# Kernel tuning notes

Hardware: AMD Instinct MI355X
Metric: run time of the kernel (lower is better)

Reference implementation:

```python
import jax, jax.numpy as jnp
import numpy as np
from jax import lax

B, T_CAP, V, WD, H, L, IC = 256, 51, 10000, 512, 512, 2, 2048


def setup_inputs() -> dict:
    key = jax.random.key(0)
    ks = jax.random.split(key, 16)
    u01 = lambda k, s: jax.random.uniform(k, s, jnp.float32, -0.1, 0.1)
    sc = 1.0 / np.sqrt(H)
    uh = lambda k, s: jax.random.uniform(k, s, jnp.float32, -sc, sc)
    image_code = jax.random.normal(ks[0], (B, IC), jnp.float32)
    captions = jax.random.randint(ks[1], (B, T_CAP), 0, V)
    cap_lens = jax.random.randint(ks[2], (B,), 2, T_CAP + 1)
    cap_lens = cap_lens.at[0].set(T_CAP)  # guarantees max len == T_CAP (static scan length)
    return {
        "image_code": image_code,
        "captions": captions,
        "cap_lens": cap_lens,
        "embed_w": u01(ks[3], (V, WD)),
        "init_w": uh(ks[4], (L * H, IC)),
        "init_b": uh(ks[5], (L * H,)),
        "w_ih0": uh(ks[6], (3 * H, WD + IC)),
        "w_hh0": uh(ks[7], (3 * H, H)),
        "b_ih0": uh(ks[8], (3 * H,)),
        "b_hh0": uh(ks[9], (3 * H,)),
        "w_ih1": uh(ks[10], (3 * H, H)),
        "w_hh1": uh(ks[11], (3 * H, H)),
        "b_ih1": uh(ks[12], (3 * H,)),
        "b_hh1": uh(ks[13], (3 * H,)),
        "fc_w": u01(ks[14], (V, H)),
        "fc_b": jnp.zeros((V,), jnp.float32),
    }


def _gru_cell(x, h, w_ih, w_hh, b_ih, b_hh):
    # torch nn.GRU cell: gates ordered (r, z, n)
    gi = x @ w_ih.T + b_ih
    gh = h @ w_hh.T + b_hh
    i_r, i_z, i_n = jnp.split(gi, 3, axis=-1)
    h_r, h_z, h_n = jnp.split(gh, 3, axis=-1)
    r = jax.nn.sigmoid(i_r + h_r)
    z = jax.nn.sigmoid(i_z + h_z)
    n = jnp.tanh(i_n + r * h_n)
    return (1.0 - z) * n + z * h


def reference(image_code, captions, cap_lens, embed_w, init_w, init_b,
              w_ih0, w_hh0, b_ih0, b_hh0, w_ih1, w_hh1, b_ih1, b_hh1,
              fc_w, fc_b):
    b = image_code.shape[0]
    # sort by caption length, descending (ragged batch shrink in original)
    order = jnp.argsort(-cap_lens)
    sorted_lens = cap_lens[order]
    caps = captions[order]
    img = image_code[order]
    # init hidden: (L, B, H)
    h0 = (img @ init_w.T + init_b).reshape(b, L, H).transpose(1, 0, 2)
    lengths = sorted_lens - 1                      # decode steps per example
    T = captions.shape[1] - 1                      # static; equals lengths[0] by construction
    emb = embed_w[caps]                            # (B, T+1, WD)
    xs = jnp.swapaxes(emb[:, :T, :], 0, 1)         # (T, B, WD)
    mask_ts = jnp.arange(T)[:, None] < lengths[None, :]  # (T, B)
    params = [(w_ih0, w_hh0, b_ih0, b_hh0), (w_ih1, w_hh1, b_ih1, b_hh1)]

    def step(h, inp):
        x_emb, m = inp
        layer_in = jnp.concatenate([img, x_emb], axis=-1)  # (B, IC+WD)
        new_h = []
        for l, (wi, wh, bi, bh) in enumerate(params):
            hl = _gru_cell(layer_in, h[l], wi, wh, bi, bh)
            new_h.append(hl)
            layer_in = hl
        h_new = jnp.stack(new_h)
        # rows past their length keep their old hidden (equivalent to the
        # torch loop never touching rows beyond real_batch_size)
        h_new = jnp.where(m[None, :, None], h_new, h)
        preds = layer_in @ fc_w.T + fc_b           # dropout is identity in eval
        preds = jnp.where(m[:, None], preds, 0.0)  # predictions stay zero past length
        return h_new, preds

    _, preds = lax.scan(step, h0, (xs, mask_ts))   # preds: (T, B, V)
    predictions = jnp.swapaxes(preds, 0, 1)        # (B, T, V)
    return predictions, caps, lengths, order
```

## Files before the change

kernel.cpp:

```cpp
#include <hip/hip_runtime.h>
#include <hip/hip_bf16.h>

#define BB   256
#define TCAP 51
#define TT   50
#define VV   10000
#define WDIM 512
#define HH   512
#define ICC  2048
#define G3H  1536
#define FCP  8

typedef __attribute__((ext_vector_type(8))) short short8v;
typedef __attribute__((ext_vector_type(4))) float f32x4;

__device__ __forceinline__ unsigned short f2bf(float f) {
    unsigned u; __builtin_memcpy(&u, &f, 4);
    unsigned r = (u + 0x7FFFu + ((u >> 16) & 1u)) >> 16;
    return (unsigned short)r;
}
__device__ __forceinline__ float bf2f(unsigned short b) {
    unsigned u = ((unsigned)b) << 16; float f; __builtin_memcpy(&f, &u, 4); return f;
}
__device__ __forceinline__ short8v cvt8(float4 a, float4 b) {
    union { unsigned short u[8]; short8v v; } o;
    o.u[0] = f2bf(a.x); o.u[1] = f2bf(a.y); o.u[2] = f2bf(a.z); o.u[3] = f2bf(a.w);
    o.u[4] = f2bf(b.x); o.u[5] = f2bf(b.y); o.u[6] = f2bf(b.z); o.u[7] = f2bf(b.w);
    return o.v;
}
__device__ __forceinline__ float sigm(float x) { return 1.f / (1.f + expf(-x)); }

__global__ void sort_kernel(const int* __restrict__ cap_lens, const int* __restrict__ captions,
                            int* __restrict__ order_ws, int* __restrict__ len_ws,
                            int* __restrict__ caps_ws, float* __restrict__ out,
                            size_t predN) {
    __shared__ int s_order[BB];
    int i = threadIdx.x;
    int li = cap_lens[i];
    int rank = 0;
    for (int j = 0; j < BB; ++j) {
        int lj = cap_lens[j];
        rank += (lj > li) || (lj == li && j < i);
    }
    s_order[rank] = i;
    __syncthreads();
    int src = s_order[i];
    order_ws[i] = src;
    int len = cap_lens[src] - 1;
    len_ws[i] = len;
    for (int t = 0; t < TCAP; ++t) {
        int c = captions[src * TCAP + t];
        caps_ws[i * TCAP + t] = c;
        out[predN + (size_t)i * TCAP + t] = (float)c;
    }
    out[predN + (size_t)BB * TCAP + i]      = (float)len;
    out[predN + (size_t)BB * TCAP + BB + i] = (float)src;
}

__global__ void gather_imgb(const float* __restrict__ image_code, const int* __restrict__ order_ws,
                            unsigned short* __restrict__ imgb) {
    int i = blockIdx.x * 256 + threadIdx.x;
    int p = i >> 8, c8 = (i & 255) << 3;
    const float* s = image_code + (size_t)order_ws[p] * ICC + c8;
    float4 v0 = *(const float4*)s, v1 = *(const float4*)(s + 4);
    *(short8v*)&imgb[(size_t)p * ICC + c8] = cvt8(v0, v1);
}

__global__ void cvt_mat(const float* __restrict__ src, int src_ld, int src_off,
                        unsigned short* __restrict__ dst, int dst_ld, int dst_off,
                        int cols, int n8) {
    int i = blockIdx.x * 256 + threadIdx.x;
    if (i < n8) {
        int cpr = cols >> 3;
        int row = i / cpr, c8 = (i - row * cpr) << 3;
        const float* s = src + (size_t)row * src_ld + src_off + c8;
        float4 v0 = *(const float4*)s, v1 = *(const float4*)(s + 4);
        *(short8v*)&dst[(size_t)row * dst_ld + dst_off + c8] = cvt8(v0, v1);
    }
}

__global__ __launch_bounds__(256) void gemm_front(
    const unsigned short* __restrict__ imgb,
    const unsigned short* __restrict__ wcomb,
    const float* __restrict__ init_b,
    const float* __restrict__ b_ih0,
    unsigned short* __restrict__ h0s0,
    unsigned short* __restrict__ h1s0,
    float* __restrict__ gi_img) {
    const int p0 = blockIdx.y * 64;
    const int c0 = blockIdx.x * 64;
    const int tid = threadIdx.x;
    __shared__ unsigned short As[64][64 + FCP], Bs[64][64 + FCP];
    const int lane = tid & 63, w = tid >> 6;
    f32x4 acc[4] = {};
    for (int k0 = 0; k0 < ICC; k0 += 64) {
#pragma unroll
        for (int v = 0; v < 2; ++v) {
            int e = tid + v * 256;
            int rr = e >> 3, kk = (e & 7) * 8;
            *(short8v*)&As[rr][kk] = *(const short8v*)&imgb[(size_t)(p0 + rr) * ICC + k0 + kk];
            *(short8v*)&Bs[rr][kk] = *(const short8v*)&wcomb[(size_t)(c0 + rr) * ICC + k0 + kk];
        }
        __syncthreads();
#pragma unroll
        for (int ks = 0; ks < 64; ks += 32) {
            short8v a = *(const short8v*)&As[w * 16 + (lane & 15)][ks + (lane >> 4) * 8];
#pragma unroll
            for (int n = 0; n < 4; ++n) {
                short8v b = *(const short8v*)&Bs[n * 16 + (lane & 15)][ks + (lane >> 4) * 8];
                acc[n] = __builtin_amdgcn_mfma_f32_16x16x32_bf16(a, b, acc[n], 0, 0, 0);
            }
        }
        __syncthreads();
    }
#pragma unroll
    for (int n = 0; n < 4; ++n) {
        int cc = c0 + n * 16 + (lane & 15);
#pragma unroll
        for (int r = 0; r < 4; ++r) {
            int pr = p0 + w * 16 + (lane >> 4) * 4 + r;
            float v = acc[n][r];
            if (cc < 1024) {
                v += init_b[cc];
                unsigned short b = f2bf(v);
                if (cc < 512) h0s0[(size_t)pr * 512 + cc] = b;
                else          h1s0[(size_t)pr * 512 + (cc - 512)] = b;
            } else {
                gi_img[(size_t)pr * G3H + (cc - 1024)] = v + b_ih0[cc - 1024];
            }
        }
    }
}

__global__ __launch_bounds__(256) void gemm_giemb(
    const unsigned short* __restrict__ embb,
    const unsigned short* __restrict__ wihe,
    const float* __restrict__ gi_img,
    const int* __restrict__ caps_ws, const int* __restrict__ len_ws,
    float* __restrict__ gi_all) {
    const int r0 = blockIdx.y * 64;
    const int t = r0 >> 8, p0 = r0 & 255;
    if (len_ws[p0] <= t) return;
    const int c0 = blockIdx.x * 64;
    const int tid = threadIdx.x;
    __shared__ unsigned short As[64][64 + FCP], Bs[64][64 + FCP];
    __shared__ int s_arow[64];
    if (tid < 64) s_arow[tid] = caps_ws[(p0 + tid) * TCAP + t];
    __syncthreads();
    const int lane = tid & 63, w = tid >> 6;
    f32x4 acc[4] = {};
    for (int k0 = 0; k0 < WDIM; k0 += 64) {
#pragma unroll
        for (int v = 0; v < 2; ++v) {
            int e = tid + v * 256;
            int rr = e >> 3, kk = (e & 7) * 8;
            *(short8v*)&As[rr][kk] = *(const short8v*)&embb[(size_t)s_arow[rr] * WDIM + k0 + kk];
            *(short8v*)&Bs[rr][kk] = *(const short8v*)&wihe[(size_t)(c0 + rr) * WDIM + k0 + kk];
        }
        __syncthreads();
#pragma unroll
        for (int ks = 0; ks < 64; ks += 32) {
            short8v a = *(const short8v*)&As[w * 16 + (lane & 15)][ks + (lane >> 4) * 8];
#pragma unroll
            for (int n = 0; n < 4; ++n) {
                short8v b = *(const short8v*)&Bs[n * 16 + (lane & 15)][ks + (lane >> 4) * 8];
                acc[n] = __builtin_amdgcn_mfma_f32_16x16x32_bf16(a, b, acc[n], 0, 0, 0);
            }
        }
        __syncthreads();
    }
#pragma unroll
    for (int n = 0; n < 4; ++n) {
        int cc = c0 + n * 16 + (lane & 15);
#pragma unroll
        for (int r = 0; r < 4; ++r) {
            int pr = p0 + w * 16 + (lane >> 4) * 4 + r;
            if (t < len_ws[pr])
                gi_all[((size_t)t * BB + pr) * G3H + cc] = acc[n][r] + gi_img[(size_t)pr * G3H + cc];
        }
    }
}

__global__ __launch_bounds__(256, 1) void gru_stage(int s,
    const unsigned short* __restrict__ h0_rd, unsigned short* __restrict__ h0_wr,
    float* __restrict__ gx_wr, const float* __restrict__ gx_rd,
    const unsigned short* __restrict__ h1_rd, unsigned short* __restrict__ h1_wr,
    unsigned short* __restrict__ h1x,
    const unsigned short* __restrict__ whh0b,
    const unsigned short* __restrict__ wih1b,
    const unsigned short* __restrict__ whh1b,
    const float* __restrict__ b_hh0, const float* __restrict__ gi_all,
    const float* __restrict__ b_ih1, const float* __restrict__ b_hh1,
    const int* __restrict__ len_ws) {
    const int role = blockIdx.x >> 5;
    const int sub = blockIdx.x & 31;
    const int cc0 = (sub & 7) * 64;
    const int p0 = (sub >> 3) * 64;
    const int t = s - role;
    if (t < 0 || t >= TT) return;
    if (len_ws[p0] <= t) return;
    const int tid = threadIdx.x, lane = tid & 63, w = tid >> 6;
    __shared__ unsigned short Bs[2][3][64][72];
    const unsigned short* Arows = (role == 2) ? h1_rd : h0_rd;
    const unsigned short* Bw = (role == 0) ? whh0b : (role == 1) ? wih1b : whh1b;
    const int rr0 = tid >> 3, kk0 = (tid & 7) * 8;

    const int arow = p0 + w * 16 + (lane & 15);
    const int akoff = (lane >> 4) * 8;
    short8v af[16];
#pragma unroll
    for (int kc = 0; kc < 8; ++kc) {
        af[kc * 2]     = *(const short8v*)&Arows[(size_t)arow * 512 + kc * 64 + akoff];
        af[kc * 2 + 1] = *(const short8v*)&Arows[(size_t)arow * 512 + kc * 64 + 32 + akoff];
    }

    f32x4 aG0[4] = {}, aG1[4] = {}, aG2[4] = {};
    short8v pb[2][6];

#define LOADB(SL, KC) {                                                              \
    size_t ko = (size_t)(KC) * 64 + kk0;                                             \
    pb[SL][0] = *(const short8v*)&Bw[(size_t)(cc0 + rr0) * 512 + ko];                \
    pb[SL][1] = *(const short8v*)&Bw[(size_t)(cc0 + rr0 + 32) * 512 + ko];           \
    pb[SL][2] = *(const short8v*)&Bw[(size_t)(512 + cc0 + rr0) * 512 + ko];          \
    pb[SL][3] = *(const short8v*)&Bw[(size_t)(512 + cc0 + rr0 + 32) * 512 + ko];     \
    pb[SL][4] = *(const short8v*)&Bw[(size_t)(1024 + cc0 + rr0) * 512 + ko];         \
    pb[SL][5] = *(const short8v*)&Bw[(size_t)(1024 + cc0 + rr0 + 32) * 512 + ko]; }

    LOADB(0, 0);
    LOADB(1, 1);
#pragma unroll
    for (int kc = 0; kc < 8; ++kc) {
        const int sl = kc & 1;
        *(short8v*)&Bs[sl][0][rr0][kk0]      = pb[sl][0];
        *(short8v*)&Bs[sl][0][rr0 + 32][kk0] = pb[sl][1];
        *(short8v*)&Bs[sl][1][rr0][kk0]      = pb[sl][2];
        *(short8v*)&Bs[sl][1][rr0 + 32][kk0] = pb[sl][3];
        *(short8v*)&Bs[sl][2][rr0][kk0]      = pb[sl][4];
        *(short8v*)&Bs[sl][2][rr0 + 32][kk0] = pb[sl][5];
        __syncthreads();
        if (kc < 6) LOADB(sl, kc + 2);
#pragma unroll
        for (int ks = 0; ks < 2; ++ks) {
            short8v a = af[kc * 2 + ks];
#pragma unroll
            for (int n = 0; n < 4; ++n) {
                int br = n * 16 + (lane & 15), bk = ks * 32 + (lane >> 4) * 8;
                short8v b0 = *(const short8v*)&Bs[sl][0][br][bk];
                aG0[n] = __builtin_amdgcn_mfma_f32_16x16x32_bf16(a, b0, aG0[n], 0, 0, 0);
                short8v b1 = *(const short8v*)&Bs[sl][1][br][bk];
                aG1[n] = __builtin_amdgcn_mfma_f32_16x16x32_bf16(a, b1, aG1[n], 0, 0, 0);
                short8v b2 = *(const short8v*)&Bs[sl][2][br][bk];
                aG2[n] = __builtin_amdgcn_mfma_f32_16x16x32_bf16(a, b2, aG2[n], 0, 0, 0);
            }
        }
    }
#undef LOADB

    if (role == 0) {
#pragma unroll
        for (int n = 0; n < 4; ++n) {
            int cc = cc0 + n * 16 + (lane & 15);
            float bR = b_hh0[cc], bZ = b_hh0[512 + cc], bN = b_hh0[1024 + cc];
#pragma unroll
            for (int r = 0; r < 4; ++r) {
                int p = p0 + w * 16 + (lane >> 4) * 4 + r;
                const float* gi = gi_all + ((size_t)t * BB + p) * G3H;
                float rr_ = sigm(gi[cc] + aG0[n][r] + bR);
                float zz  = sigm(gi[512 + cc] + aG1[n][r] + bZ);
                float nn  = tanhf(gi[1024 + cc] + rr_ * (aG2[n][r] + bN));
                float hold = bf2f(h0_rd[(size_t)p * 512 + cc]);
                float hnew = (t < len_ws[p]) ? (1.f - zz) * nn + zz * hold : hold;
                h0_wr[(size_t)p * 512 + cc] = f2bf(hnew);
            }
        }
    } else if (role == 1) {
#pragma unroll
        for (int n = 0; n < 4; ++n) {
            int cc = cc0 + n * 16 + (lane & 15);
            float bR = b_ih1[cc], bZ = b_ih1[512 + cc], bN = b_ih1[1024 + cc];
#pragma unroll
            for (int r = 0; r < 4; ++r) {
                int p = p0 + w * 16 + (lane >> 4) * 4 + r;
                float* gx = gx_wr + (size_t)p * G3H;
                gx[cc]        = aG0[n][r] + bR;
                gx[512 + cc]  = aG1[n][r] + bZ;
                gx[1024 + cc] = aG2[n][r] + bN;
            }
        }
    } else {
#pragma unroll
        for (int n = 0; n < 4; ++n) {
            int cc = cc0 + n * 16 + (lane & 15);
            float bR = b_hh1[cc], bZ = b_hh1[512 + cc], bN = b_hh1[1024 + cc];
#pragma unroll
            for (int r = 0; r < 4; ++r) {
                int p = p0 + w * 16 + (lane >> 4) * 4 + r;
                const float* gx = gx_rd + (size_t)p * G3H;
                float rr_ = sigm(gx[cc] + aG0[n][r] + bR);
                float zz  = sigm(gx[512 + cc] + aG1[n][r] + bZ);
                float nn  = tanhf(gx[1024 + cc] + rr_ * (aG2[n][r] + bN));
                float hold = bf2f(h1_rd[(size_t)p * 512 + cc]);
                float hnew = (t < len_ws[p]) ? (1.f - zz) * nn + zz * hold : hold;
                unsigned short hb = f2bf(hnew);
                h1_wr[(size_t)p * 512 + cc] = hb;
                h1x[((size_t)t * BB + p) * 512 + cc] = hb;
            }
        }
    }
}

__global__ __launch_bounds__(256) void gemm_fc_mfma(
    const unsigned short* __restrict__ h1x,
    const unsigned short* __restrict__ fcwb,
    const float* __restrict__ fc_b,
    const int* __restrict__ len_ws,
    float* __restrict__ out) {
    const int r0 = blockIdx.y * 64;
    const int t = r0 >> 8, p0 = r0 & 255;
    const int c0 = blockIdx.x * 64;
    const int tid = threadIdx.x;
    if (len_ws[p0] <= t) {
        for (int e = tid; e < 64 * 16; e += 256) {
            int rl = e >> 4, c = c0 + (e & 15) * 4;
            if (c < VV) {
                float4 z = {0.f, 0.f, 0.f, 0.f};
                *(float4*)&out[((size_t)(p0 + rl) * TT + t) * VV + c] = z;
            }
        }
        return;
    }
    __shared__ unsigned short As[64][64 + FCP];
    __shared__ unsigned short Bs[64][64 + FCP];
    const int lane = tid & 63, w = tid >> 6;
    f32x4 acc[4] = {};
    for (int k0 = 0; k0 < HH; k0 += 64) {
#pragma unroll
        for (int v = 0; v < 2; ++v) {
            int e = tid + v * 256;
            int rr = e >> 3, kk = (e & 7) * 8;
            *(short8v*)&As[rr][kk] =
                *(const short8v*)&h1x[((size_t)(t * BB + p0 + rr)) * HH + k0 + kk];
            int bc = c0 + rr;
            short8v bv = {};
            if (bc < VV) bv = *(const short8v*)&fcwb[(size_t)bc * HH + k0 + kk];
            *(short8v*)&Bs[rr][kk] = bv;
        }
        __syncthreads();
#pragma unroll
        for (int ks = 0; ks < 64; ks += 32) {
            short8v a = *(const short8v*)&As[w * 16 + (lane & 15)][ks + (lane >> 4) * 8];
#pragma unroll
            for (int n = 0; n < 4; ++n) {
                short8v b = *(const short8v*)&Bs[n * 16 + (lane & 15)][ks + (lane >> 4) * 8];
                acc[n] = __builtin_amdgcn_mfma_f32_16x16x32_bf16(a, b, acc[n], 0, 0, 0);
            }
        }
        __syncthreads();
    }
#pragma unroll
    for (int n = 0; n < 4; ++n) {
        int c = c0 + n * 16 + (lane & 15);
        if (c < VV) {
            float bias = fc_b[c];
#pragma unroll
            for (int r = 0; r < 4; ++r) {
                int pr = p0 + w * 16 + (lane >> 4) * 4 + r;
                bool act = (t < len_ws[pr]);
                out[((size_t)pr * TT + t) * VV + c] = act ? (acc[n][r] + bias) : 0.f;
            }
        }
    }
}

extern "C" void kernel_launch(void* const* d_in, const int* in_sizes, int n_in,
                              void* d_out, int out_size, void* d_ws, size_t ws_size,
                              hipStream_t stream) {
    const float* image_code = (const float*)d_in[0];
    const int*   captions   = (const int*)d_in[1];
    const int*   cap_lens   = (const int*)d_in[2];
    const float* embed_w    = (const float*)d_in[3];
    const float* init_w     = (const float*)d_in[4];
    const float* init_b     = (const float*)d_in[5];
    const float* w_ih0      = (const float*)d_in[6];
    const float* w_hh0      = (const float*)d_in[7];
    const float* b_ih0      = (const float*)d_in[8];
    const float* b_hh0      = (const float*)d_in[9];
    const float* w_ih1      = (const float*)d_in[10];
    const float* w_hh1      = (const float*)d_in[11];
    const float* b_ih1      = (const float*)d_in[12];
    const float* b_hh1      = (const float*)d_in[13];
    const float* fc_w       = (const float*)d_in[14];
    const float* fc_b       = (const float*)d_in[15];
    float* out = (float*)d_out;

    const size_t tail = (size_t)BB * TCAP + 2 * BB;
    const size_t predN = (size_t)out_size - tail;

    char* ws = (char*)d_ws;
    int*   order_ws = (int*)(ws + 0);
    int*   len_ws   = (int*)(ws + 1024);
    int*   caps_ws  = (int*)(ws + 2048);
    unsigned short* h0s[2] = {(unsigned short*)(ws + 54272),  (unsigned short*)(ws + 316416)};
    unsigned short* h1s[2] = {(unsigned short*)(ws + 578560), (unsigned short*)(ws + 840704)};
    float* gxb[2] = {(float*)(ws + 1102848), (float*)(ws + 2675712)};
    float* gi_img   = (float*)(ws + 4248576);
    float* gi_all   = (float*)(ws + 5821440);
    unsigned short* h1x  = (unsigned short*)(ws + 84464640);
    unsigned short* fcwb = (unsigned short*)(ws + 97571840);

    char* ob = (char*)d_out;
    unsigned short* imgb   = (unsigned short*)(ob + 0);
    unsigned short* wihe   = (unsigned short*)(ob + 1048576);
    unsigned short* wcomb  = (unsigned short*)(ob + 4194304);
    unsigned short* embb   = (unsigned short*)(ob + 16777216);
    unsigned short* whh0b  = (unsigned short*)(ob + 27262976);
    unsigned short* wih1b  = (unsigned short*)(ob + 29360128);
    unsigned short* whh1b  = (unsigned short*)(ob + 31457280);

    dim3 blk(256);
    hipLaunchKernelGGL(sort_kernel, dim3(1), blk, 0, stream,
                       cap_lens, captions, order_ws, len_ws, caps_ws, out, predN);
    hipLaunchKernelGGL(gather_imgb, dim3(256), blk, 0, stream, image_code, order_ws, imgb);
    hipLaunchKernelGGL(cvt_mat, dim3(1024), blk, 0, stream,
                       init_w, ICC, 0, wcomb, ICC, 0, ICC, 1024 * ICC / 8);
    hipLaunchKernelGGL(cvt_mat, dim3(1536), blk, 0, stream,
                       w_ih0, ICC + WDIM, 0, wcomb + (size_t)1024 * ICC, ICC, 0, ICC, G3H * ICC / 8);
    hipLaunchKernelGGL(cvt_mat, dim3(384), blk, 0, stream,
                       w_ih0, ICC + WDIM, ICC, wihe, WDIM, 0, WDIM, G3H * WDIM / 8);
    hipLaunchKernelGGL(cvt_mat, dim3(2500), blk, 0, stream,
                       embed_w, WDIM, 0, embb, WDIM, 0, WDIM, VV * WDIM / 8);
    hipLaunchKernelGGL(cvt_mat, dim3(2500), blk, 0, stream,
                       fc_w, WDIM, 0, fcwb, WDIM, 0, WDIM, VV * WDIM / 8);
    hipLaunchKernelGGL(cvt_mat, dim3(384), blk, 0, stream,
                       w_hh0, WDIM, 0, whh0b, WDIM, 0, WDIM, G3H * WDIM / 8);
    hipLaunchKernelGGL(cvt_mat, dim3(384), blk, 0, stream,
                       w_ih1, WDIM, 0, wih1b, WDIM, 0, WDIM, G3H * WDIM / 8);
    hipLaunchKernelGGL(cvt_mat, dim3(384), blk, 0, stream,
                       w_hh1, WDIM, 0, whh1b, WDIM, 0, WDIM, G3H * WDIM / 8);

    hipLaunchKernelGGL(gemm_front, dim3(40, 4), blk, 0, stream,
                       imgb, wcomb, init_b, b_ih0, h0s[0], h1s[0], gi_img);
    hipLaunchKernelGGL(gemm_giemb, dim3(24, 200), blk, 0, stream,
                       embb, wihe, gi_img, caps_ws, len_ws, gi_all);

    for (int s = 0; s <= TT + 1; ++s) {
        int q = s & 1;
        hipLaunchKernelGGL(gru_stage, dim3(96), blk, 0, stream, s,
                           h0s[q], h0s[q ^ 1],
                           gxb[q ^ 1], gxb[q],
                           h1s[q], h1s[q ^ 1],
                           h1x, whh0b, wih1b, whh1b,
                           b_hh0, gi_all, b_ih1, b_hh1, len_ws);
    }

    hipLaunchKernelGGL(gemm_fc_mfma, dim3(157, 200), blk, 0, stream,
                       h1x, fcwb, fc_b, len_ws, out);
}
```

Measured before the change: 1.253 ms.

## Fuse FC projection into pipelined GRU stage launches, overlapping with recurrence

```diff
diff --git a/kernel.cpp b/kernel.cpp
--- a/kernel.cpp
+++ b/kernel.cpp
@@ -181,7 +181,7 @@
     }
 }
 
-__global__ __launch_bounds__(256, 1) void gru_stage(int s,
+__global__ __launch_bounds__(256, 1) void gru_fc_stage(int s,
     const unsigned short* __restrict__ h0_rd, unsigned short* __restrict__ h0_wr,
     float* __restrict__ gx_wr, const float* __restrict__ gx_rd,
     const unsigned short* __restrict__ h1_rd, unsigned short* __restrict__ h1_wr,
@@ -191,31 +191,39 @@
     const unsigned short* __restrict__ whh1b,
     const float* __restrict__ b_hh0, const float* __restrict__ gi_all,
     const float* __restrict__ b_ih1, const float* __restrict__ b_hh1,
+    const unsigned short* __restrict__ fcwb,
+    const float* __restrict__ fc_b,
+    float* __restrict__ out,
     const int* __restrict__ len_ws) {
-    const int role = blockIdx.x >> 5;
-    const int sub = blockIdx.x & 31;
-    const int cc0 = (sub & 7) * 64;
-    const int p0 = (sub >> 3) * 64;
-    const int t = s - role;
-    if (t < 0 || t >= TT) return;
-    if (len_ws[p0] <= t) return;
+    __shared__ __align__(16) unsigned char smem_raw[55296];
+    const int bid = blockIdx.x;
     const int tid = threadIdx.x, lane = tid & 63, w = tid >> 6;
-    __shared__ unsigned short Bs[2][3][64][72];
-    const unsigned short* Arows = (role == 2) ? h1_rd : h0_rd;
-    const unsigned short* Bw = (role == 0) ? whh0b : (role == 1) ? wih1b : whh1b;
-    const int rr0 = tid >> 3, kk0 = (tid & 7) * 8;
-
-    const int arow = p0 + w * 16 + (lane & 15);
-    const int akoff = (lane >> 4) * 8;
-    short8v af[16];
-#pragma unroll
-    for (int kc = 0; kc < 8; ++kc) {
-        af[kc * 2]     = *(const short8v*)&Arows[(size_t)arow * 512 + kc * 64 + akoff];
-        af[kc * 2 + 1] = *(const short8v*)&Arows[(size_t)arow * 512 + kc * 64 + 32 + akoff];
-    }
-
-    f32x4 aG0[4] = {}, aG1[4] = {}, aG2[4] = {};
-    short8v pb[2][6];
+
+    if (bid < 96) {
+        const int role = bid >> 5;
+        const int sub = bid & 31;
+        const int cc0 = (sub & 7) * 64;
+        const int p0 = (sub >> 3) * 64;
+        const int t = s - role;
+        if (t < 0 || t >= TT) return;
+        if (len_ws[p0] <= t) return;
+        unsigned short (*Bs)[3][64][72] =
+            reinterpret_cast<unsigned short (*)[3][64][72]>(smem_raw);
+        const unsigned short* Arows = (role == 2) ? h1_rd : h0_rd;
+        const unsigned short* Bw = (role == 0) ? whh0b : (role == 1) ? wih1b : whh1b;
+        const int rr0 = tid >> 3, kk0 = (tid & 7) * 8;
+
+        const int arow = p0 + w * 16 + (lane & 15);
+        const int akoff = (lane >> 4) * 8;
+        short8v af[16];
+#pragma unroll
+        for (int kc = 0; kc < 8; ++kc) {
+            af[kc * 2]     = *(const short8v*)&Arows[(size_t)arow * 512 + kc * 64 + akoff];
+            af[kc * 2 + 1] = *(const short8v*)&Arows[(size_t)arow * 512 + kc * 64 + 32 + akoff];
+        }
+
+        f32x4 aG0[4] = {}, aG1[4] = {}, aG2[4] = {};
+        short8v pb[2][6];
 
 #define LOADB(SL, KC) {                                                              \
     size_t ko = (size_t)(KC) * 64 + kk0;                                             \
@@ -226,99 +234,95 @@
     pb[SL][4] = *(const short8v*)&Bw[(size_t)(1024 + cc0 + rr0) * 512 + ko];         \
     pb[SL][5] = *(const short8v*)&Bw[(size_t)(1024 + cc0 + rr0 + 32) * 512 + ko]; }
 
-    LOADB(0, 0);
-    LOADB(1, 1);
-#pragma unroll
-    for (int kc = 0; kc < 8; ++kc) {
-        const int sl = kc & 1;
-        *(short8v*)&Bs[sl][0][rr0][kk0]      = pb[sl][0];
-        *(short8v*)&Bs[sl][0][rr0 + 32][kk0] = pb[sl][1];
-        *(short8v*)&Bs[sl][1][rr0][kk0]      = pb[sl][2];
-        *(short8v*)&Bs[sl][1][rr0 + 32][kk0] = pb[sl][3];
-        *(short8v*)&Bs[sl][2][rr0][kk0]      = pb[sl][4];
-        *(short8v*)&Bs[sl][2][rr0 + 32][kk0] = pb[sl][5];
-        __syncthreads();
-        if (kc < 6) LOADB(sl, kc + 2);
-#pragma unroll
-        for (int ks = 0; ks < 2; ++ks) {
-            short8v a = af[kc * 2 + ks];
-#pragma unroll
-            for (int n = 0; n < 4; ++n) {
-                int br = n * 16 + (lane & 15), bk = ks * 32 + (lane >> 4) * 8;
-                short8v b0 = *(const short8v*)&Bs[sl][0][br][bk];
-                aG0[n] = __builtin_amdgcn_mfma_f32_16x16x32_bf16(a, b0, aG0[n], 0, 0, 0);
-                short8v b1 = *(const short8v*)&Bs[sl][1][br][bk];
-                aG1[n] = __builtin_amdgcn_mfma_f32_16x16x32_bf16(a, b1, aG1[n], 0, 0, 0);
-                short8v b2 = *(const short8v*)&Bs[sl][2][br][bk];
-                aG2[n] = __builtin_amdgcn_mfma_f32_16x16x32_bf16(a, b2, aG2[n], 0, 0, 0);
-            }
-        }
-    }
+        LOADB(0, 0);
+        LOADB(1, 1);
+#pragma unroll
+        for (int kc = 0; kc < 8; ++kc) {
+            const int sl = kc & 1;
+            *(short8v*)&Bs[sl][0][rr0][kk0]      = pb[sl][0];
+            *(short8v*)&Bs[sl][0][rr0 + 32][kk0] = pb[sl][1];
+            *(short8v*)&Bs[sl][1][rr0][kk0]      = pb[sl][2];
+            *(short8v*)&Bs[sl][1][rr0 + 32][kk0] = pb[sl][3];
+            *(short8v*)&Bs[sl][2][rr0][kk0]      = pb[sl][4];
+            *(short8v*)&Bs[sl][2][rr0 + 32][kk0] = pb[sl][5];
+            __syncthreads();
+            if (kc < 6) LOADB(sl, kc + 2);
+#pragma unroll
+            for (int ks = 0; ks < 2; ++ks) {
+                short8v a = af[kc * 2 + ks];
+#pragma unroll
+                for (int n = 0; n < 4; ++n) {
+                    int br = n * 16 + (lane & 15), bk = ks * 32 + (lane >> 4) * 8;
+                    short8v b0 = *(const short8v*)&Bs[sl][0][br][bk];
+                    aG0[n] = __builtin_amdgcn_mfma_f32_16x16x32_bf16(a, b0, aG0[n], 0, 0, 0);
+                    short8v b1 = *(const short8v*)&Bs[sl][1][br][bk];
+                    aG1[n] = __builtin_amdgcn_mfma_f32_16x16x32_bf16(a, b1, aG1[n], 0, 0, 0);
+                    short8v b2 = *(const short8v*)&Bs[sl][2][br][bk];
+                    aG2[n] = __builtin_amdgcn_mfma_f32_16x16x32_bf16(a, b2, aG2[n], 0, 0, 0);
+                }
+            }
+        }
 #undef LOADB
 
-    if (role == 0) {
-#pragma unroll
-        for (int n = 0; n < 4; ++n) {
-            int cc = cc0 + n * 16 + (lane & 15);
-            float bR = b_hh0[cc], bZ = b_hh0[512 + cc], bN = b_hh0[1024 + cc];
-#pragma unroll
-            for (int r = 0; r < 4; ++r) {
-                int p = p0 + w * 16 + (lane >> 4) * 4 + r;
-                const float* gi = gi_all + ((size_t)t * BB + p) * G3H;
-                float rr_ = sigm(gi[cc] + aG0[n][r] + bR);
-                float zz  = sigm(gi[512 + cc] + aG1[n][r] + bZ);
-                float nn  = tanhf(gi[1024 + cc] + rr_ * (aG2[n][r] + bN));
-                float hold = bf2f(h0_rd[(size_t)p * 512 + cc]);
-                float hnew = (t < len_ws[p]) ? (1.f - zz) * nn + zz * hold : hold;
-                h0_wr[(size_t)p * 512 + cc] = f2bf(hnew);
-            }
-        }
-    } else if (role == 1) {
-#pragma unroll
-        for (int n = 0; n < 4; ++n) {
-            int cc = cc0 + n * 16 + (lane & 15);
-            float bR = b_ih1[cc], bZ = b_ih1[512 + cc], bN = b_ih1[1024 + cc];
-#pragma unroll
-            for (int r = 0; r < 4; ++r) {
-                int p = p0 + w * 16 + (lane >> 4) * 4 + r;
-                float* gx = gx_wr + (size_t)p * G3H;
-                gx[cc]        = aG0[n][r] + bR;
-                gx[512 + cc]  = aG1[n][r] + bZ;
-                gx[1024 + cc] = aG2[n][r] + bN;
-            }
-        }
-    } else {
-#pragma unroll
-        for (int n = 0; n < 4; ++n) {
-            int cc = cc0 + n * 16 + (lane & 15);
-            float bR = b_hh1[cc], bZ = b_hh1[512 + cc], bN = b_hh1[1024 + cc];
-#pragma unroll
-            for (int r = 0; r < 4; ++r) {
-                int p = p0 + w * 16 + (lane >> 4) * 4 + r;
-                const float* gx = gx_rd + (size_t)p * G3H;
-                float rr_ = sigm(gx[cc] + aG0[n][r] + bR);
-                float zz  = sigm(gx[512 + cc] + aG1[n][r] + bZ);
-                float nn  = tanhf(gx[1024 + cc] + rr_ * (aG2[n][r] + bN));
-                float hold = bf2f(h1_rd[(size_t)p * 512 + cc]);
-                float hnew = (t < len_ws[p]) ? (1.f - zz) * nn + zz * hold : hold;
-                unsigned short hb = f2bf(hnew);
-                h1_wr[(size_t)p * 512 + cc] = hb;
-                h1x[((size_t)t * BB + p) * 512 + cc] = hb;
-            }
-        }
-    }
-}
-
-__global__ __launch_bounds__(256) void gemm_fc_mfma(
-    const unsigned short* __restrict__ h1x,
-    const unsigned short* __restrict__ fcwb,
-    const float* __restrict__ fc_b,
-    const int* __restrict__ len_ws,
-    float* __restrict__ out) {
-    const int r0 = blockIdx.y * 64;
-    const int t = r0 >> 8, p0 = r0 & 255;
-    const int c0 = blockIdx.x * 64;
-    const int tid = threadIdx.x;
+        if (role == 0) {
+#pragma unroll
+            for (int n = 0; n < 4; ++n) {
+                int cc = cc0 + n * 16 + (lane & 15);
+                float bR = b_hh0[cc], bZ = b_hh0[512 + cc], bN = b_hh0[1024 + cc];
+#pragma unroll
+                for (int r = 0; r < 4; ++r) {
+                    int p = p0 + w * 16 + (lane >> 4) * 4 + r;
+                    const float* gi = gi_all + ((size_t)t * BB + p) * G3H;
+                    float rr_ = sigm(gi[cc] + aG0[n][r] + bR);
+                    float zz  = sigm(gi[512 + cc] + aG1[n][r] + bZ);
+                    float nn  = tanhf(gi[1024 + cc] + rr_ * (aG2[n][r] + bN));
+                    float hold = bf2f(h0_rd[(size_t)p * 512 + cc]);
+                    float hnew = (t < len_ws[p]) ? (1.f - zz) * nn + zz * hold : hold;
+                    h0_wr[(size_t)p * 512 + cc] = f2bf(hnew);
+                }
+            }
+        } else if (role == 1) {
+#pragma unroll
+            for (int n = 0; n < 4; ++n) {
+                int cc = cc0 + n * 16 + (lane & 15);
+                float bR = b_ih1[cc], bZ = b_ih1[512 + cc], bN = b_ih1[1024 + cc];
+#pragma unroll
+                for (int r = 0; r < 4; ++r) {
+                    int p = p0 + w * 16 + (lane >> 4) * 4 + r;
+                    float* gx = gx_wr + (size_t)p * G3H;
+                    gx[cc]        = aG0[n][r] + bR;
+                    gx[512 + cc]  = aG1[n][r] + bZ;
+                    gx[1024 + cc] = aG2[n][r] + bN;
+                }
+            }
+        } else {
+#pragma unroll
+            for (int n = 0; n < 4; ++n) {
+                int cc = cc0 + n * 16 + (lane & 15);
+                float bR = b_hh1[cc], bZ = b_hh1[512 + cc], bN = b_hh1[1024 + cc];
+#pragma unroll
+                for (int r = 0; r < 4; ++r) {
+                    int p = p0 + w * 16 + (lane >> 4) * 4 + r;
+                    const float* gx = gx_rd + (size_t)p * G3H;
+                    float rr_ = sigm(gx[cc] + aG0[n][r] + bR);
+                    float zz  = sigm(gx[512 + cc] + aG1[n][r] + bZ);
+                    float nn  = tanhf(gx[1024 + cc] + rr_ * (aG2[n][r] + bN));
+                    float hold = bf2f(h1_rd[(size_t)p * 512 + cc]);
+                    float hnew = (t < len_ws[p]) ? (1.f - zz) * nn + zz * hold : hold;
+                    unsigned short hb = f2bf(hnew);
+                    h1_wr[(size_t)p * 512 + cc] = hb;
+                    h1x[((size_t)t * BB + p) * 512 + cc] = hb;
+                }
+            }
+        }
+        return;
+    }
+
+    const int t = s - 3;
+    if (t < 0 || t >= TT) return;
+    const int idx = bid - 96;
+    const int c0 = (idx % 157) * 64;
+    const int p0 = (idx / 157) * 64;
     if (len_ws[p0] <= t) {
         for (int e = tid; e < 64 * 16; e += 256) {
             int rl = e >> 4, c = c0 + (e & 15) * 4;
@@ -329,9 +333,9 @@
         }
         return;
     }
-    __shared__ unsigned short As[64][64 + FCP];
-    __shared__ unsigned short Bs[64][64 + FCP];
-    const int lane = tid & 63, w = tid >> 6;
+    unsigned short (*As)[64 + FCP] = reinterpret_cast<unsigned short (*)[64 + FCP]>(smem_raw);
+    unsigned short (*Bsf)[64 + FCP] =
+        reinterpret_cast<unsigned short (*)[64 + FCP]>(smem_raw + 64 * (64 + FCP) * 2);
     f32x4 acc[4] = {};
     for (int k0 = 0; k0 < HH; k0 += 64) {
 #pragma unroll
@@ -343,7 +347,7 @@
             int bc = c0 + rr;
             short8v bv = {};
             if (bc < VV) bv = *(const short8v*)&fcwb[(size_t)bc * HH + k0 + kk];
-            *(short8v*)&Bs[rr][kk] = bv;
+            *(short8v*)&Bsf[rr][kk] = bv;
         }
         __syncthreads();
 #pragma unroll
@@ -351,7 +355,7 @@
             short8v a = *(const short8v*)&As[w * 16 + (lane & 15)][ks + (lane >> 4) * 8];
 #pragma unroll
             for (int n = 0; n < 4; ++n) {
-                short8v b = *(const short8v*)&Bs[n * 16 + (lane & 15)][ks + (lane >> 4) * 8];
+                short8v b = *(const short8v*)&Bsf[n * 16 + (lane & 15)][ks + (lane >> 4) * 8];
                 acc[n] = __builtin_amdgcn_mfma_f32_16x16x32_bf16(a, b, acc[n], 0, 0, 0);
             }
         }
@@ -416,6 +420,10 @@
     unsigned short* whh0b  = (unsigned short*)(ob + 27262976);
     unsigned short* wih1b  = (unsigned short*)(ob + 29360128);
     unsigned short* whh1b  = (unsigned short*)(ob + 31457280);
+    unsigned short* whh0b_s = (unsigned short*)(ws + 110000128);
+    unsigned short* wih1b_s = (unsigned short*)(ws + 111572992);
+    unsigned short* whh1b_s = (unsigned short*)(ws + 113145856);
+    (void)whh0b; (void)wih1b; (void)whh1b;
 
     dim3 blk(256);
     hipLaunchKernelGGL(sort_kernel, dim3(1), blk, 0, stream,
@@ -432,27 +440,25 @@
     hipLaunchKernelGGL(cvt_mat, dim3(2500), blk, 0, stream,
                        fc_w, WDIM, 0, fcwb, WDIM, 0, WDIM, VV * WDIM / 8);
     hipLaunchKernelGGL(cvt_mat, dim3(384), blk, 0, stream,
-                       w_hh0, WDIM, 0, whh0b, WDIM, 0, WDIM, G3H * WDIM / 8);
+                       w_hh0, WDIM, 0, whh0b_s, WDIM, 0, WDIM, G3H * WDIM / 8);
     hipLaunchKernelGGL(cvt_mat, dim3(384), blk, 0, stream,
-                       w_ih1, WDIM, 0, wih1b, WDIM, 0, WDIM, G3H * WDIM / 8);
+                       w_ih1, WDIM, 0, wih1b_s, WDIM, 0, WDIM, G3H * WDIM / 8);
     hipLaunchKernelGGL(cvt_mat, dim3(384), blk, 0, stream,
-                       w_hh1, WDIM, 0, whh1b, WDIM, 0, WDIM, G3H * WDIM / 8);
+                       w_hh1, WDIM, 0, whh1b_s, WDIM, 0, WDIM, G3H * WDIM / 8);
 
     hipLaunchKernelGGL(gemm_front, dim3(40, 4), blk, 0, stream,
                        imgb, wcomb, init_b, b_ih0, h0s[0], h1s[0], gi_img);
     hipLaunchKernelGGL(gemm_giemb, dim3(24, 200), blk, 0, stream,
                        embb, wihe, gi_img, caps_ws, len_ws, gi_all);
 
-    for (int s = 0; s <= TT + 1; ++s) {
+    for (int s = 0; s <= TT + 2; ++s) {
         int q = s & 1;
-        hipLaunchKernelGGL(gru_stage, dim3(96), blk, 0, stream, s,
+        hipLaunchKernelGGL(gru_fc_stage, dim3(96 + 628), blk, 0, stream, s,
                            h0s[q], h0s[q ^ 1],
                            gxb[q ^ 1], gxb[q],
                            h1s[q], h1s[q ^ 1],
-                           h1x, whh0b, wih1b, whh1b,
-                           b_hh0, gi_all, b_ih1, b_hh1, len_ws);
-    }
-
-    hipLaunchKernelGGL(gemm_fc_mfma, dim3(157, 200), blk, 0, stream,
-                       h1x, fcwb, fc_b, len_ws, out);
-}
+                           h1x, whh0b_s, wih1b_s, whh1b_s,
+                           b_hh0, gi_all, b_ih1, b_hh1,
+                           fcwb, fc_b, out, len_ws);
+    }
+}
```

New measurement: 1.243 ms. Within noise of the previous version (-0.8%).
